# Optimization experiments

Hardware: AMD Instinct MI355X
Metric: run time of the kernel (lower is better)

## Reference

```python
import jax, jax.numpy as jnp
import numpy as np

N_NODES = 50000
N_EDGES = 640000
IN_CH = 128
OUT_CH = 128


def setup_inputs() -> dict:
    key = jax.random.key(0)
    k1, k2, k3, k4 = jax.random.split(key, 4)
    x = jax.random.normal(k1, (N_NODES, IN_CH), dtype=jnp.float32)
    edge_index = jax.random.randint(k2, (2, N_EDGES), 0, N_NODES, dtype=jnp.int32)
    # nn.Linear params: W [out, in], b [out]
    bound = 1.0 / np.sqrt(IN_CH)
    W = jax.random.uniform(k3, (OUT_CH, IN_CH), minval=-bound, maxval=bound, dtype=jnp.float32)
    b = jax.random.uniform(k4, (OUT_CH,), minval=-bound, maxval=bound, dtype=jnp.float32)
    return {"x": x, "edge_index": edge_index, "W": W, "b": b}


def reference(x, edge_index, W, b):
    row, col = edge_index[0], edge_index[1]
    num_nodes = x.shape[0]
    # degree of each destination node (clamped to >= 1)
    deg = jax.ops.segment_sum(jnp.ones(row.shape[0], dtype=x.dtype), row,
                              num_segments=num_nodes)
    deg = jnp.maximum(deg, 1.0)
    # gather neighbor features and scatter-add into destinations
    agg = jax.ops.segment_sum(x[col], row, num_segments=num_nodes)
    agg = agg / deg[:, None]
    # residual + linear
    return (x + agg) @ W.T + b
```

## Files before the change

### kernel.cpp

```cpp
#include <hip/hip_runtime.h>

#define N_NODES 50000
#define N_EDGES 640000
#define CH 128
#define CAP 48

typedef __bf16 bf16_t;
typedef bf16_t bf16x8 __attribute__((ext_vector_type(8)));
typedef float f32x4 __attribute__((ext_vector_type(4)));

__device__ __forceinline__ ushort f2bf(float f) {
  union { float f; unsigned u; } v; v.f = f;
  unsigned r = v.u + 0x7FFFu + ((v.u >> 16) & 1u);
  return (ushort)(r >> 16);
}
__device__ __forceinline__ float bflo(unsigned u) {
  union { unsigned u; float f; } v; v.u = u << 16; return v.f;
}
__device__ __forceinline__ float bfhi(unsigned u) {
  union { unsigned u; float f; } v; v.u = u & 0xFFFF0000u; return v.f;
}
__device__ __forceinline__ unsigned pack2(float lo, float hi) {
  return (unsigned)f2bf(lo) | ((unsigned)f2bf(hi) << 16);
}


__global__ __launch_bounds__(256) void prep(const float4* __restrict__ x4,
                                            const float4* __restrict__ W4,
                                            uint4* __restrict__ xb4,
                                            uint4* __restrict__ Wb4,
                                            int4* __restrict__ cnt4) {
  int i = blockIdx.x * 256 + threadIdx.x;
  float4 a = x4[i * 2], b = x4[i * 2 + 1];
  uint4 o;
  o.x = pack2(a.x, a.y); o.y = pack2(a.z, a.w);
  o.z = pack2(b.x, b.y); o.w = pack2(b.z, b.w);
  xb4[i] = o;
  if (i < 2048) {
    float4 c = W4[i * 2], d = W4[i * 2 + 1];
    uint4 w;
    w.x = pack2(c.x, c.y); w.y = pack2(c.z, c.w);
    w.z = pack2(d.x, d.y); w.w = pack2(d.z, d.w);
    Wb4[i] = w;
  }
  if (i < 12500) cnt4[i] = make_int4(0, 0, 0, 0);
}

__global__ __launch_bounds__(256) void fill(const int* __restrict__ row,
                                            const int* __restrict__ col,
                                            int* __restrict__ cnt,
                                            ushort* __restrict__ adj) {
  int t = blockIdx.x * 256 + threadIdx.x;
  int4 r4 = *(const int4*)(row + t * 4);
  int4 c4 = *(const int4*)(col + t * 4);
  int p0 = atomicAdd(&cnt[r4.x], 1);
  int p1 = atomicAdd(&cnt[r4.y], 1);
  int p2 = atomicAdd(&cnt[r4.z], 1);
  int p3 = atomicAdd(&cnt[r4.w], 1);
  if (p0 < CAP) adj[r4.x * CAP + p0] = (ushort)c4.x;
  if (p1 < CAP) adj[r4.y * CAP + p1] = (ushort)c4.y;
  if (p2 < CAP) adj[r4.z * CAP + p2] = (ushort)c4.z;
  if (p3 < CAP) adj[r4.w * CAP + p3] = (ushort)c4.w;
}

__global__ __launch_bounds__(512) void fused(const uint4* __restrict__ xb4,
                                             const int* __restrict__ cnt,
                                             const ushort* __restrict__ adj,
                                             const uint4* __restrict__ Wb4,
                                             const float4* __restrict__ bias4,
                                             float4* __restrict__ out4) {
  __shared__ ushort hT[64 * CH];
  int tid = threadIdx.x;
  int wv = tid >> 6;
  int lane = tid & 63;
  int q = lane & 15;
  int grp = lane >> 4;
  int m0 = blockIdx.x * 64;

#pragma unroll
  for (int t = 0; t < 2; ++t) {
    int r = wv * 8 + t * 4 + grp;
    int node = m0 + r;
    int deg = 0;
    if (node < N_NODES) deg = cnt[node];
    int degc = deg < CAP ? deg : CAP;
    const ushort* arow = adj + node * CAP;
    float acc[8] = {0.f, 0.f, 0.f, 0.f, 0.f, 0.f, 0.f, 0.f};
    int e = 0;
    for (; e + 3 < degc; e += 4) {
      uint2 ids = *(const uint2*)(arow + e);
      int n0 = ids.x & 0xFFFF, n1 = ids.x >> 16;
      int n2 = ids.y & 0xFFFF, n3 = ids.y >> 16;
      uint4 v0 = xb4[n0 * 16 + q];
      uint4 v1 = xb4[n1 * 16 + q];
      uint4 v2 = xb4[n2 * 16 + q];
      uint4 v3 = xb4[n3 * 16 + q];
      acc[0] += bflo(v0.x); acc[1] += bfhi(v0.x); acc[2] += bflo(v0.y); acc[3] += bfhi(v0.y);
      acc[4] += bflo(v0.z); acc[5] += bfhi(v0.z); acc[6] += bflo(v0.w); acc[7] += bfhi(v0.w);
      acc[0] += bflo(v1.x); acc[1] += bfhi(v1.x); acc[2] += bflo(v1.y); acc[3] += bfhi(v1.y);
      acc[4] += bflo(v1.z); acc[5] += bfhi(v1.z); acc[6] += bflo(v1.w); acc[7] += bfhi(v1.w);
      acc[0] += bflo(v2.x); acc[1] += bfhi(v2.x); acc[2] += bflo(v2.y); acc[3] += bfhi(v2.y);
      acc[4] += bflo(v2.z); acc[5] += bfhi(v2.z); acc[6] += bflo(v2.w); acc[7] += bfhi(v2.w);
      acc[0] += bflo(v3.x); acc[1] += bfhi(v3.x); acc[2] += bflo(v3.y); acc[3] += bfhi(v3.y);
      acc[4] += bflo(v3.z); acc[5] += bfhi(v3.z); acc[6] += bflo(v3.w); acc[7] += bfhi(v3.w);
    }
    for (; e < degc; ++e) {
      int nb = arow[e];
      uint4 v = xb4[nb * 16 + q];
      acc[0] += bflo(v.x); acc[1] += bfhi(v.x); acc[2] += bflo(v.y); acc[3] += bfhi(v.y);
      acc[4] += bflo(v.z); acc[5] += bfhi(v.z); acc[6] += bflo(v.w); acc[7] += bfhi(v.w);
    }
    uint4 o = make_uint4(0, 0, 0, 0);
    if (node < N_NODES) {
      float s = 1.0f / fmaxf((float)deg, 1.0f);
      uint4 xi = xb4[node * 16 + q];
      o.x = pack2(bflo(xi.x) + acc[0] * s, bfhi(xi.x) + acc[1] * s);
      o.y = pack2(bflo(xi.y) + acc[2] * s, bfhi(xi.y) + acc[3] * s);
      o.z = pack2(bflo(xi.z) + acc[4] * s, bfhi(xi.z) + acc[5] * s);
      o.w = pack2(bflo(xi.w) + acc[6] * s, bfhi(xi.w) + acc[7] * s);
    }
    *(uint4*)&hT[r * CH + q * 8] = o;
  }
  __syncthreads();

  int qq = grp;
  int mt = wv & 3;
  int nbase = (wv >> 2) * 4;
  const ushort* hrow = &hT[(mt * 16 + q) * CH + qq * 8];
  bf16x8 hb0 = *(const bf16x8*)(hrow);
  bf16x8 hb1 = *(const bf16x8*)(hrow + 32);
  bf16x8 hb2 = *(const bf16x8*)(hrow + 64);
  bf16x8 hb3 = *(const bf16x8*)(hrow + 96);
  int m = m0 + mt * 16 + q;
#pragma unroll
  for (int i = 0; i < 4; ++i) {
    int nt = nbase + i;
    const uint4* wr = Wb4 + (nt * 16 + q) * 16 + qq;
    bf16x8 w0 = __builtin_bit_cast(bf16x8, wr[0]);
    bf16x8 w1 = __builtin_bit_cast(bf16x8, wr[4]);
    bf16x8 w2 = __builtin_bit_cast(bf16x8, wr[8]);
    bf16x8 w3 = __builtin_bit_cast(bf16x8, wr[12]);
    f32x4 acc = {0.f, 0.f, 0.f, 0.f};
    acc = __builtin_amdgcn_mfma_f32_16x16x32_bf16(w0, hb0, acc, 0, 0, 0);
    acc = __builtin_amdgcn_mfma_f32_16x16x32_bf16(w1, hb1, acc, 0, 0, 0);
    acc = __builtin_amdgcn_mfma_f32_16x16x32_bf16(w2, hb2, acc, 0, 0, 0);
    acc = __builtin_amdgcn_mfma_f32_16x16x32_bf16(w3, hb3, acc, 0, 0, 0);
    if (m < N_NODES) {
      float4 bv = bias4[nt * 4 + qq];
      float4 o;
      o.x = acc[0] + bv.x;
      o.y = acc[1] + bv.y;
      o.z = acc[2] + bv.z;
      o.w = acc[3] + bv.w;
      out4[(size_t)m * 32 + nt * 4 + qq] = o;
    }
  }
}

extern "C" void kernel_launch(void* const* d_in, const int* in_sizes, int n_in,
                              void* d_out, int out_size, void* d_ws, size_t ws_size,
                              hipStream_t stream) {
  const float* x  = (const float*)d_in[0];
  const int*   ei = (const int*)d_in[1];
  const float* W  = (const float*)d_in[2];
  const float* bb = (const float*)d_in[3];

  char* ws = (char*)d_ws;
  int*    cnt = (int*)ws;
  ushort* adj = (ushort*)(ws + 200064);
  uint4*  Wb4 = (uint4*)(ws + 5000064);
  uint4*  xb4 = (uint4*)(ws + 5032832);

  prep<<<3125, 256, 0, stream>>>((const float4*)x, (const float4*)W,
                                 xb4, Wb4, (int4*)cnt);
  fill<<<625, 256, 0, stream>>>(ei, ei + N_EDGES, cnt, adj);
  fused<<<(N_NODES + 63) / 64, 512, 0, stream>>>(xb4, cnt, adj, Wb4,
                                                 (const float4*)bb,
                                                 (float4*)d_out);
}
```

Before: 155.8 us.

## Overlap x bf16 conversion with edge fill and pad degree counters to 64 bytes

Moves the x-to-bf16 conversion out of the prep kernel and into the edge fill kernel as extra blocks, so the atomic-heavy adjacency build and the bandwidth-bound conversion run at the same time. The prep kernel now only zeroes counters and converts W. Degree counters are spaced 16 ints apart so each node's atomic counter sits on its own 64-byte line, reducing contention between neighbouring nodes. In exchange, the counter array grows 16x, so there is more memory to zero and sparser counter reads in the fused kernel.

```diff
diff --git a/kernel.cpp b/kernel.cpp
--- a/kernel.cpp
+++ b/kernel.cpp
@@ -4,6 +4,7 @@
 #define N_EDGES 640000
 #define CH 128
 #define CAP 48
+#define CSTR 16
 
 typedef __bf16 bf16_t;
 typedef bf16_t bf16x8 __attribute__((ext_vector_type(8)));
@@ -25,17 +26,11 @@
 }
 
 
-__global__ __launch_bounds__(256) void prep(const float4* __restrict__ x4,
-                                            const float4* __restrict__ W4,
-                                            uint4* __restrict__ xb4,
+__global__ __launch_bounds__(256) void init(const float4* __restrict__ W4,
                                             uint4* __restrict__ Wb4,
                                             int4* __restrict__ cnt4) {
   int i = blockIdx.x * 256 + threadIdx.x;
-  float4 a = x4[i * 2], b = x4[i * 2 + 1];
-  uint4 o;
-  o.x = pack2(a.x, a.y); o.y = pack2(a.z, a.w);
-  o.z = pack2(b.x, b.y); o.w = pack2(b.z, b.w);
-  xb4[i] = o;
+  if (i < 200000) cnt4[i] = make_int4(0, 0, 0, 0);
   if (i < 2048) {
     float4 c = W4[i * 2], d = W4[i * 2 + 1];
     uint4 w;
@@ -43,24 +38,35 @@
     w.z = pack2(d.x, d.y); w.w = pack2(d.z, d.w);
     Wb4[i] = w;
   }
-  if (i < 12500) cnt4[i] = make_int4(0, 0, 0, 0);
 }
 
-__global__ __launch_bounds__(256) void fill(const int* __restrict__ row,
-                                            const int* __restrict__ col,
-                                            int* __restrict__ cnt,
-                                            ushort* __restrict__ adj) {
-  int t = blockIdx.x * 256 + threadIdx.x;
-  int4 r4 = *(const int4*)(row + t * 4);
-  int4 c4 = *(const int4*)(col + t * 4);
-  int p0 = atomicAdd(&cnt[r4.x], 1);
-  int p1 = atomicAdd(&cnt[r4.y], 1);
-  int p2 = atomicAdd(&cnt[r4.z], 1);
-  int p3 = atomicAdd(&cnt[r4.w], 1);
-  if (p0 < CAP) adj[r4.x * CAP + p0] = (ushort)c4.x;
-  if (p1 < CAP) adj[r4.y * CAP + p1] = (ushort)c4.y;
-  if (p2 < CAP) adj[r4.z * CAP + p2] = (ushort)c4.z;
-  if (p3 < CAP) adj[r4.w * CAP + p3] = (ushort)c4.w;
+__global__ __launch_bounds__(256) void fill_conv(const int* __restrict__ row,
+                                                 const int* __restrict__ col,
+                                                 int* __restrict__ cnt,
+                                                 ushort* __restrict__ adj,
+                                                 const float4* __restrict__ x4,
+                                                 uint4* __restrict__ xb4) {
+  int bid = blockIdx.x;
+  if (bid < 625) {
+    int t = bid * 256 + threadIdx.x;
+    int4 r4 = *(const int4*)(row + t * 4);
+    int4 c4 = *(const int4*)(col + t * 4);
+    int p0 = atomicAdd(&cnt[r4.x * CSTR], 1);
+    int p1 = atomicAdd(&cnt[r4.y * CSTR], 1);
+    int p2 = atomicAdd(&cnt[r4.z * CSTR], 1);
+    int p3 = atomicAdd(&cnt[r4.w * CSTR], 1);
+    if (p0 < CAP) adj[r4.x * CAP + p0] = (ushort)c4.x;
+    if (p1 < CAP) adj[r4.y * CAP + p1] = (ushort)c4.y;
+    if (p2 < CAP) adj[r4.z * CAP + p2] = (ushort)c4.z;
+    if (p3 < CAP) adj[r4.w * CAP + p3] = (ushort)c4.w;
+  } else {
+    int i = (bid - 625) * 256 + threadIdx.x;
+    float4 a = x4[i * 2], b = x4[i * 2 + 1];
+    uint4 o;
+    o.x = pack2(a.x, a.y); o.y = pack2(a.z, a.w);
+    o.z = pack2(b.x, b.y); o.w = pack2(b.z, b.w);
+    xb4[i] = o;
+  }
 }
 
 __global__ __launch_bounds__(512) void fused(const uint4* __restrict__ xb4,
@@ -82,7 +88,7 @@
     int r = wv * 8 + t * 4 + grp;
     int node = m0 + r;
     int deg = 0;
-    if (node < N_NODES) deg = cnt[node];
+    if (node < N_NODES) deg = cnt[node * CSTR];
     int degc = deg < CAP ? deg : CAP;
     const ushort* arow = adj + node * CAP;
     float acc[8] = {0.f, 0.f, 0.f, 0.f, 0.f, 0.f, 0.f, 0.f};
@@ -167,13 +173,13 @@
 
   char* ws = (char*)d_ws;
   int*    cnt = (int*)ws;
-  ushort* adj = (ushort*)(ws + 200064);
-  uint4*  Wb4 = (uint4*)(ws + 5000064);
-  uint4*  xb4 = (uint4*)(ws + 5032832);
+  ushort* adj = (ushort*)(ws + 3200000);
+  uint4*  Wb4 = (uint4*)(ws + 8000000);
+  uint4*  xb4 = (uint4*)(ws + 8032768);
 
-  prep<<<3125, 256, 0, stream>>>((const float4*)x, (const float4*)W,
-                                 xb4, Wb4, (int4*)cnt);
-  fill<<<625, 256, 0, stream>>>(ei, ei + N_EDGES, cnt, adj);
+  init<<<782, 256, 0, stream>>>((const float4*)W, Wb4, (int4*)cnt);
+  fill_conv<<<3750, 256, 0, stream>>>(ei, ei + N_EDGES, cnt, adj,
+                                      (const float4*)x, xb4);
   fused<<<(N_NODES + 63) / 64, 512, 0, stream>>>(xb4, cnt, adj, Wb4,
                                                  (const float4*)bb,
                                                  (float4*)d_out);
```

Result: no change. 157.7 us (+1.2%).
